# Kernel optimization log

Measured on AMD Instinct MI355X. Metric: run time of the kernel, lower is better.

The kernel has to match this reference:

```python
import jax, jax.numpy as jnp
import numpy as np

ALPHA = 1.702   # GLU sigmoid scale
LIMIT = 7.0     # clamp limit
K = 2           # experts per token


def setup_inputs() -> dict:
    key = jax.random.key(0)
    ks = jax.random.split(key, 4)
    B, S, H, E, I = 1, 1024, 1024, 8, 1024
    return {
        "hidden_states": jax.random.normal(ks[0], (B, S, H), jnp.float32),
        "router_weight": jax.random.normal(ks[1], (E, H), jnp.float32),
        "router_bias": jnp.zeros((E,), jnp.float32),
        "gate_up_proj": jax.random.normal(ks[2], (E, H, 2 * I), jnp.float32) * 0.02,
        "gate_up_bias": jnp.zeros((E, 2 * I), jnp.float32),
        "down_proj": jax.random.normal(ks[3], (E, I, H), jnp.float32) * 0.02,
        "down_bias": jnp.zeros((E, H), jnp.float32),
    }


def reference(hidden_states, router_weight, router_bias, gate_up_proj,
              gate_up_bias, down_proj, down_bias):
    B, S, H = hidden_states.shape
    E = router_weight.shape[0]
    I = down_proj.shape[1]
    T = B * S

    flat = hidden_states.reshape(T, H)

    # Router: softmax over experts, top-K selection (weights NOT renormalized).
    logits = flat @ router_weight.T + router_bias               # [T, E]
    scores = jax.nn.softmax(logits, axis=-1)
    topk_vals, topk_idx = jax.lax.top_k(scores, K)              # [T, K]

    # Dense per-token expert weight matrix (equivalent of dispatch metadata +
    # combine * topk_weights in the tt pipeline); top-k indices are unique.
    w = jnp.zeros((T, E), scores.dtype).at[
        jnp.arange(T)[:, None], topk_idx].set(topk_vals)        # [T, E]

    # Expert MLP with clamped GLU (gpt-oss style).
    gu = jnp.einsum('th,ehf->tef', flat, gate_up_proj) + gate_up_bias  # [T,E,2I]
    gate = jnp.minimum(gu[..., :I], LIMIT)
    up = jnp.clip(gu[..., I:], -LIMIT, LIMIT)
    glu = gate * jax.nn.sigmoid(gate * ALPHA)
    act = (up + 1.0) * glu                                       # [T, E, I]

    down = jnp.einsum('tei,eih->teh', act, down_proj) + down_bias  # [T, E, H]

    # Weighted combine over selected experts.
    out = jnp.einsum('teh,te->th', down, w)
    return out.reshape(B, S, H)
```

## Files before the change

kernel.cpp:

```cpp
#include <hip/hip_runtime.h>
#include <hip/hip_bf16.h>


typedef unsigned short u16;
typedef __attribute__((ext_vector_type(8))) __bf16 bf16x8;
typedef __attribute__((ext_vector_type(4))) float f32x4;

#define T_TOK 1024
#define H_DIM 1024
#define E_NUM 8
#define I_DIM 1024
#define ALPHA 1.702f
#define LIMIT 7.0f

__device__ __forceinline__ u16 f2bf(float f) {
    unsigned u = __builtin_bit_cast(unsigned, f);
    u = (u + 0x7FFFu + ((u >> 16) & 1u)) >> 16;
    return (u16)u;
}

__device__ __forceinline__ unsigned pk2(float lo, float hi) {
#if defined(__has_builtin) && __has_builtin(__builtin_amdgcn_cvt_pk_bf16_f32)
    typedef __attribute__((ext_vector_type(2))) __bf16 bf16x2_t;
    bf16x2_t v = __builtin_amdgcn_cvt_pk_bf16_f32(lo, hi);
    return __builtin_bit_cast(unsigned, v);
#else
    return (unsigned)f2bf(lo) | ((unsigned)f2bf(hi) << 16);
#endif
}

__device__ __forceinline__ f32x4 mfma16(bf16x8 a, bf16x8 b, f32x4 c) {
    return __builtin_amdgcn_mfma_f32_16x16x32_bf16(a, b, c, 0, 0, 0);
}

__device__ __forceinline__ void gld16(const void* g, void* l) {
    __builtin_amdgcn_global_load_lds(
        (const __attribute__((address_space(1))) void*)g,
        (__attribute__((address_space(3))) void*)l, 16, 0, 0);
}

__device__ __forceinline__ void expert_range(const int* counts, int e,
                                             int& cnt, int& abase) {
    int a = 0, c = 0;
#pragma unroll
    for (int i = 0; i < E_NUM; ++i) {
        int v = counts[i];
        if (i < e) a += v;
        if (i == e) c = v;
    }
    cnt = c; abase = a;
}

__global__ __launch_bounds__(256) void k_cvt(
    const float* __restrict__ gup, const float* __restrict__ dp,
    u16* __restrict__ gupT, u16* __restrict__ dpT, int* __restrict__ counts)
{
    if (blockIdx.x == 0 && threadIdx.x < E_NUM) counts[threadIdx.x] = 0;
    const int b = blockIdx.x;
    const float* src; u16* dst; int C, k0, c0;
    if (b < 4096) {
        int e = b >> 9, t = b & 511;
        k0 = (t >> 5) * 64; c0 = (t & 31) * 64;
        src = gup + ((size_t)e << 21); dst = gupT + ((size_t)e << 21); C = 2048;
    } else {
        int b2 = b - 4096;
        int e = b2 >> 8, t = b2 & 255;
        k0 = (t >> 4) * 64; c0 = (t & 15) * 64;
        src = dp + ((size_t)e << 20); dst = dpT + ((size_t)e << 20); C = 1024;
    }
    __shared__ u16 Ls[64][72];
    const int tid = threadIdx.x;
    const int rr = tid >> 4, cc = (tid & 15) * 4;
#pragma unroll
    for (int i = 0; i < 4; ++i) {
        int k = rr + i * 16;
        float4 v = *(const float4*)(src + (size_t)(k0 + k) * C + c0 + cc);
        Ls[cc + 0][k] = f2bf(v.x);
        Ls[cc + 1][k] = f2bf(v.y);
        Ls[cc + 2][k] = f2bf(v.z);
        Ls[cc + 3][k] = f2bf(v.w);
    }
    __syncthreads();
    const int oc = tid >> 2, och = (tid & 3) * 16;
    u16* orow = dst + (size_t)(c0 + oc) * 1024 + k0 + och;
    *(uint4*)(orow)     = *(uint4*)&Ls[oc][och];
    *(uint4*)(orow + 8) = *(uint4*)&Ls[oc][och + 8];
}

__global__ __launch_bounds__(256) void k_router(
    const float* __restrict__ x, const float* __restrict__ rw,
    const float* __restrict__ rb, const float* __restrict__ db,
    int* __restrict__ counts, int* __restrict__ tok_list,
    float* __restrict__ w_list, u16* __restrict__ xb,
    float* __restrict__ out)
{
    const int t = blockIdx.x;
    const int tid = threadIdx.x;
    const float4 xv = *(const float4*)(x + (size_t)t * H_DIM + tid * 4);

    *(uint2*)(xb + (size_t)t * H_DIM + tid * 4) =
        make_uint2(pk2(xv.x, xv.y), pk2(xv.z, xv.w));

    float p[E_NUM];
#pragma unroll
    for (int e = 0; e < E_NUM; ++e) {
        const float4 wv = *(const float4*)(rw + e * H_DIM + tid * 4);
        p[e] = xv.x * wv.x + xv.y * wv.y + xv.z * wv.z + xv.w * wv.w;
    }
#pragma unroll
    for (int off = 32; off; off >>= 1) {
#pragma unroll
        for (int e = 0; e < E_NUM; ++e) p[e] += __shfl_down(p[e], off, 64);
    }
    __shared__ float red[4][E_NUM];
    __shared__ int se[2];
    __shared__ float sw[2];
    const int lane = tid & 63, wvid = tid >> 6;
    if (lane == 0) {
#pragma unroll
        for (int e = 0; e < E_NUM; ++e) red[wvid][e] = p[e];
    }
    __syncthreads();
    if (tid == 0) {
        float lg[E_NUM];
#pragma unroll
        for (int e = 0; e < E_NUM; ++e)
            lg[e] = red[0][e] + red[1][e] + red[2][e] + red[3][e] + rb[e];
        float m1 = -1e30f, m2 = -1e30f; int i1 = 0, i2 = 0;
#pragma unroll
        for (int e = 0; e < E_NUM; ++e) {
            float l = lg[e];
            if (l > m1) { m2 = m1; i2 = i1; m1 = l; i1 = e; }
            else if (l > m2) { m2 = l; i2 = e; }
        }
        float s = 0.f;
#pragma unroll
        for (int e = 0; e < E_NUM; ++e) s += __expf(lg[e] - m1);
        const float w0 = 1.0f / s;
        const float w1 = __expf(m2 - m1) / s;
        int slot0 = atomicAdd(&counts[i1], 1);
        tok_list[i1 * T_TOK + slot0] = t;
        w_list[i1 * T_TOK + slot0] = w0;
        int slot1 = atomicAdd(&counts[i2], 1);
        tok_list[i2 * T_TOK + slot1] = t;
        w_list[i2 * T_TOK + slot1] = w1;
        se[0] = i1; se[1] = i2; sw[0] = w0; sw[1] = w1;
    }
    __syncthreads();
    const int e0 = se[0], e1 = se[1];
    const float w0 = sw[0], w1 = sw[1];
    const int c = tid * 4;
    float4 d0 = *(const float4*)(db + e0 * H_DIM + c);
    float4 d1 = *(const float4*)(db + e1 * H_DIM + c);
    float4 o;
    o.x = w0 * d0.x + w1 * d1.x;
    o.y = w0 * d0.y + w1 * d1.y;
    o.z = w0 * d0.z + w1 * d1.z;
    o.w = w0 * d0.w + w1 * d1.w;
    *(float4*)(out + (size_t)t * H_DIM + c) = o;
}

__global__ __launch_bounds__(256, 4) void k_gateup(
    const u16* __restrict__ gupT, const float* __restrict__ gub,
    const int* __restrict__ counts, const int* __restrict__ tok_list,
    const u16* __restrict__ xb, u16* __restrict__ act)
{
    const int e = blockIdx.z;
    int cnt, abase;
    expert_range(counts, e, cnt, abase);
    const int m0 = blockIdx.y * 64;
    if (m0 >= cnt) return;
    const int n0 = blockIdx.x * 32;
    const int tid = threadIdx.x;
    const int lane = tid & 63, wv = tid >> 6;
    const int fm = lane & 15, kg = lane >> 4;
    const int wm = wv >> 1, wn = wv & 1;

    __shared__ __align__(16) u16 As0[64 * 64], As1[64 * 64];
    __shared__ __align__(16) u16 Bs0[64 * 64], Bs1[64 * 64];

    const int lr = lane >> 3, lk = (lane & 7) * 8;
    const u16* gA[2];
#pragma unroll
    for (int i = 0; i < 2; ++i) {
        int row = (wv * 2 + i) * 8 + lr;
        int slot = m0 + row;
        int tok = (slot < cnt) ? tok_list[e * T_TOK + slot] : 0;
        gA[i] = xb + (size_t)tok * H_DIM + lk;
    }
    const u16* gB[2];
#pragma unroll
    for (int i = 0; i < 2; ++i) {
        int row = (wv * 2 + i) * 8 + lr;
        int col = (row < 32) ? (n0 + row) : (1024 + n0 + row - 32);
        gB[i] = gupT + ((size_t)e << 21) + (size_t)col * 1024 + lk;
    }

    f32x4 accg[2], accu[2];
#pragma unroll
    for (int m = 0; m < 2; ++m) {
        accg[m] = (f32x4){0.f, 0.f, 0.f, 0.f};
        accu[m] = (f32x4){0.f, 0.f, 0.f, 0.f};
    }

#define GU_STAGE(AS, BS, KB)                                                   \
    {                                                                          \
        gld16(gA[0] + (KB), (u16*)(AS) + (wv * 2 + 0) * 512);                  \
        gld16(gA[1] + (KB), (u16*)(AS) + (wv * 2 + 1) * 512);                  \
        gld16(gB[0] + (KB), (u16*)(BS) + (wv * 2 + 0) * 512);                  \
        gld16(gB[1] + (KB), (u16*)(BS) + (wv * 2 + 1) * 512);                  \
    }
#define GU_MFMA(AS, BS)                                                        \
    {                                                                          \
        _Pragma("unroll")                                                      \
        for (int ks = 0; ks < 2; ++ks) {                                       \
            const int ko = ks * 32 + kg * 8;                                   \
            bf16x8 a0 = *(const bf16x8*)((const u16*)(AS) + (wm * 32 + fm) * 64 + ko);      \
            bf16x8 a1 = *(const bf16x8*)((const u16*)(AS) + (wm * 32 + 16 + fm) * 64 + ko); \
            bf16x8 bg = *(const bf16x8*)((const u16*)(BS) + (wn * 16 + fm) * 64 + ko);      \
            bf16x8 bu = *(const bf16x8*)((const u16*)(BS) + (32 + wn * 16 + fm) * 64 + ko); \
            accg[0] = mfma16(a0, bg, accg[0]);                                 \
            accu[0] = mfma16(a0, bu, accu[0]);                                 \
            accg[1] = mfma16(a1, bg, accg[1]);                                 \
            accu[1] = mfma16(a1, bu, accu[1]);                                 \
        }                                                                      \
    }

    GU_STAGE(As0, Bs0, 0);
    __syncthreads();
    for (int kb = 0; kb < H_DIM; kb += 128) {
        GU_STAGE(As1, Bs1, kb + 64);
        GU_MFMA(As0, Bs0);
        __syncthreads();
        if (kb + 128 < H_DIM) GU_STAGE(As0, Bs0, kb + 128);
        GU_MFMA(As1, Bs1);
        __syncthreads();
    }
#undef GU_STAGE
#undef GU_MFMA

#pragma unroll
    for (int m = 0; m < 2; ++m) {
#pragma unroll
        for (int r = 0; r < 4; ++r) {
            int row = wm * 32 + m * 16 + kg * 4 + r;
            int slot = m0 + row;
            if (slot >= cnt) continue;
            size_t arow = (size_t)(abase + slot) * I_DIM;
            int cn = n0 + wn * 16 + fm;
            float g = accg[m][r] + gub[e * 2048 + cn];
            float u = accu[m][r] + gub[e * 2048 + 1024 + cn];
            g = fminf(g, LIMIT);
            u = fminf(fmaxf(u, -LIMIT), LIMIT);
            float glu = g / (1.f + __expf(-ALPHA * g));
            act[arow + cn] = f2bf((u + 1.f) * glu);
        }
    }
}

__global__ __launch_bounds__(256, 4) void k_down(
    const u16* __restrict__ dpT,
    const int* __restrict__ counts, const int* __restrict__ tok_list,
    const float* __restrict__ w_list,
    const u16* __restrict__ act, float* __restrict__ out)
{
    const int e = blockIdx.z & 7, ks = blockIdx.z >> 3;
    int cnt, abase;
    expert_range(counts, e, cnt, abase);
    const int m0 = blockIdx.y * 64;
    if (m0 >= cnt) return;
    const int n0 = blockIdx.x * 64;
    const int tid = threadIdx.x;
    const int lane = tid & 63, wv = tid >> 6;
    const int fm = lane & 15, kg = lane >> 4;
    const int wm = wv >> 1, wn = wv & 1;

    __shared__ __align__(16) u16 As0[64 * 64], As1[64 * 64];
    __shared__ __align__(16) u16 Bs0[64 * 64], Bs1[64 * 64];

    const int lr = lane >> 3, lk = (lane & 7) * 8;
    const u16* gA[2];
    const u16* gB[2];
#pragma unroll
    for (int i = 0; i < 2; ++i) {
        int row = (wv * 2 + i) * 8 + lr;
        gA[i] = act + (size_t)(abase + m0 + row) * I_DIM + ks * 512 + lk;
        gB[i] = dpT + ((size_t)e << 20) + (size_t)(n0 + row) * 1024 + ks * 512 + lk;
    }

    f32x4 acc[2][2];
#pragma unroll
    for (int m = 0; m < 2; ++m)
#pragma unroll
        for (int n = 0; n < 2; ++n) acc[m][n] = (f32x4){0.f, 0.f, 0.f, 0.f};

#define DN_STAGE(AS, BS, KB)                                                   \
    {                                                                          \
        gld16(gA[0] + (KB), (u16*)(AS) + (wv * 2 + 0) * 512);                  \
        gld16(gA[1] + (KB), (u16*)(AS) + (wv * 2 + 1) * 512);                  \
        gld16(gB[0] + (KB), (u16*)(BS) + (wv * 2 + 0) * 512);                  \
        gld16(gB[1] + (KB), (u16*)(BS) + (wv * 2 + 1) * 512);                  \
    }
#define DN_MFMA(AS, BS)                                                        \
    {                                                                          \
        _Pragma("unroll")                                                      \
        for (int ks2 = 0; ks2 < 2; ++ks2) {                                    \
            const int ko = ks2 * 32 + kg * 8;                                  \
            bf16x8 a0 = *(const bf16x8*)((const u16*)(AS) + (wm * 32 + fm) * 64 + ko);      \
            bf16x8 a1 = *(const bf16x8*)((const u16*)(AS) + (wm * 32 + 16 + fm) * 64 + ko); \
            bf16x8 b0 = *(const bf16x8*)((const u16*)(BS) + (wn * 32 + fm) * 64 + ko);      \
            bf16x8 b1 = *(const bf16x8*)((const u16*)(BS) + (wn * 32 + 16 + fm) * 64 + ko); \
            acc[0][0] = mfma16(a0, b0, acc[0][0]);                             \
            acc[0][1] = mfma16(a0, b1, acc[0][1]);                             \
            acc[1][0] = mfma16(a1, b0, acc[1][0]);                             \
            acc[1][1] = mfma16(a1, b1, acc[1][1]);                             \
        }                                                                      \
    }

    DN_STAGE(As0, Bs0, 0);
    __syncthreads();
    for (int kb = 0; kb < 512; kb += 128) {
        DN_STAGE(As1, Bs1, kb + 64);
        DN_MFMA(As0, Bs0);
        __syncthreads();
        if (kb + 128 < 512) DN_STAGE(As0, Bs0, kb + 128);
        DN_MFMA(As1, Bs1);
        __syncthreads();
    }
#undef DN_STAGE
#undef DN_MFMA

#pragma unroll
    for (int m = 0; m < 2; ++m) {
#pragma unroll
        for (int r = 0; r < 4; ++r) {
            int row = wm * 32 + m * 16 + kg * 4 + r;
            int slot = m0 + row;
            if (slot >= cnt) continue;
            float wgt = w_list[e * T_TOK + slot];
            int tok = tok_list[e * T_TOK + slot];
            float* orow = out + (size_t)tok * H_DIM;
#pragma unroll
            for (int n = 0; n < 2; ++n) {
                int col = n0 + wn * 32 + n * 16 + fm;
                atomicAdd(orow + col, acc[m][n][r] * wgt);
            }
        }
    }
}

extern "C" void kernel_launch(void* const* d_in, const int* in_sizes, int n_in,
                              void* d_out, int out_size, void* d_ws, size_t ws_size,
                              hipStream_t stream) {
    const float* x   = (const float*)d_in[0];
    const float* rw  = (const float*)d_in[1];
    const float* rb  = (const float*)d_in[2];
    const float* gup = (const float*)d_in[3];
    const float* gub = (const float*)d_in[4];
    const float* dp  = (const float*)d_in[5];
    const float* db  = (const float*)d_in[6];
    float* out = (float*)d_out;

    char* ws = (char*)d_ws;
    int*   counts   = (int*)(ws);
    int*   tok_list = (int*)(ws + 64);
    float* w_list   = (float*)(ws + 64 + 32768);
    u16*   xb       = (u16*)(ws + 65600);
    u16*   act      = (u16*)(ws + 65600 + 2097152);
    u16*   gupT     = (u16*)(ws + 8388608);
    u16*   dpT      = (u16*)(ws + 41943040);

    k_cvt<<<6144, 256, 0, stream>>>(gup, dp, gupT, dpT, counts);
    k_router<<<T_TOK, 256, 0, stream>>>(x, rw, rb, db, counts, tok_list, w_list,
                                        xb, out);
    k_gateup<<<dim3(32, 16, 8), 256, 0, stream>>>(gupT, gub, counts, tok_list,
                                                  xb, act);
    k_down<<<dim3(16, 16, 16), 256, 0, stream>>>(dpT, counts, tok_list, w_list,
                                                 act, out);
}
```

Before: 221.0 us.

## Widen gate-up tile, drop down-proj split-K, pack bf16 stores in convert

The gate-up kernel now computes 64 output columns per block instead of 32, which doubles the B tile and the accumulators and reuses each A fragment across more MFMAs. The launch grid is halved and the occupancy hint drops to 3. The down-projection kernel no longer splits K into two halves, so each block runs the full I reduction and fewer atomic adds hit the output. The weight-convert kernel reads four rows per thread and writes packed bf16 pairs as 8-byte shared stores instead of scalar 2-byte stores. The trade-off is lower parallelism in gate-up and down, and more registers and shared memory per block.

```diff
diff --git a/kernel.cpp b/kernel.cpp
--- a/kernel.cpp
+++ b/kernel.cpp
@@ -68,17 +68,19 @@
         k0 = (t >> 4) * 64; c0 = (t & 15) * 64;
         src = dp + ((size_t)e << 20); dst = dpT + ((size_t)e << 20); C = 1024;
     }
-    __shared__ u16 Ls[64][72];
+    __shared__ __align__(16) u16 Ls[64][72];
     const int tid = threadIdx.x;
-    const int rr = tid >> 4, cc = (tid & 15) * 4;
+    const int kq = tid >> 4, cq = tid & 15;
+    float4 v0 = *(const float4*)(src + (size_t)(k0 + kq * 4 + 0) * C + c0 + cq * 4);
+    float4 v1 = *(const float4*)(src + (size_t)(k0 + kq * 4 + 1) * C + c0 + cq * 4);
+    float4 v2 = *(const float4*)(src + (size_t)(k0 + kq * 4 + 2) * C + c0 + cq * 4);
+    float4 v3 = *(const float4*)(src + (size_t)(k0 + kq * 4 + 3) * C + c0 + cq * 4);
+    const float* p0 = (const float*)&v0; const float* p1 = (const float*)&v1;
+    const float* p2 = (const float*)&v2; const float* p3 = (const float*)&v3;
 #pragma unroll
     for (int i = 0; i < 4; ++i) {
-        int k = rr + i * 16;
-        float4 v = *(const float4*)(src + (size_t)(k0 + k) * C + c0 + cc);
-        Ls[cc + 0][k] = f2bf(v.x);
-        Ls[cc + 1][k] = f2bf(v.y);
-        Ls[cc + 2][k] = f2bf(v.z);
-        Ls[cc + 3][k] = f2bf(v.w);
+        *(uint2*)&Ls[cq * 4 + i][kq * 4] =
+            make_uint2(pk2(p0[i], p1[i]), pk2(p2[i], p3[i]));
     }
     __syncthreads();
     const int oc = tid >> 2, och = (tid & 3) * 16;
@@ -160,7 +162,7 @@
     *(float4*)(out + (size_t)t * H_DIM + c) = o;
 }
 
-__global__ __launch_bounds__(256, 4) void k_gateup(
+__global__ __launch_bounds__(256, 3) void k_gateup(
     const u16* __restrict__ gupT, const float* __restrict__ gub,
     const int* __restrict__ counts, const int* __restrict__ tok_list,
     const u16* __restrict__ xb, u16* __restrict__ act)
@@ -170,14 +172,14 @@
     expert_range(counts, e, cnt, abase);
     const int m0 = blockIdx.y * 64;
     if (m0 >= cnt) return;
-    const int n0 = blockIdx.x * 32;
+    const int n0 = blockIdx.x * 64;
     const int tid = threadIdx.x;
     const int lane = tid & 63, wv = tid >> 6;
     const int fm = lane & 15, kg = lane >> 4;
     const int wm = wv >> 1, wn = wv & 1;
 
     __shared__ __align__(16) u16 As0[64 * 64], As1[64 * 64];
-    __shared__ __align__(16) u16 Bs0[64 * 64], Bs1[64 * 64];
+    __shared__ __align__(16) u16 Bs0[128 * 64], Bs1[128 * 64];
 
     const int lr = lane >> 3, lk = (lane & 7) * 8;
     const u16* gA[2];
@@ -188,41 +190,51 @@
         int tok = (slot < cnt) ? tok_list[e * T_TOK + slot] : 0;
         gA[i] = xb + (size_t)tok * H_DIM + lk;
     }
-    const u16* gB[2];
-#pragma unroll
-    for (int i = 0; i < 2; ++i) {
-        int row = (wv * 2 + i) * 8 + lr;
-        int col = (row < 32) ? (n0 + row) : (1024 + n0 + row - 32);
+    const u16* gB[4];
+#pragma unroll
+    for (int i = 0; i < 4; ++i) {
+        int row = (wv * 4 + i) * 8 + lr;
+        int col = (row < 64) ? (n0 + row) : (1024 + n0 + row - 64);
         gB[i] = gupT + ((size_t)e << 21) + (size_t)col * 1024 + lk;
     }
 
-    f32x4 accg[2], accu[2];
-#pragma unroll
-    for (int m = 0; m < 2; ++m) {
-        accg[m] = (f32x4){0.f, 0.f, 0.f, 0.f};
-        accu[m] = (f32x4){0.f, 0.f, 0.f, 0.f};
-    }
+    f32x4 accg[2][2], accu[2][2];
+#pragma unroll
+    for (int m = 0; m < 2; ++m)
+#pragma unroll
+        for (int n = 0; n < 2; ++n) {
+            accg[m][n] = (f32x4){0.f, 0.f, 0.f, 0.f};
+            accu[m][n] = (f32x4){0.f, 0.f, 0.f, 0.f};
+        }
 
 #define GU_STAGE(AS, BS, KB)                                                   \
     {                                                                          \
         gld16(gA[0] + (KB), (u16*)(AS) + (wv * 2 + 0) * 512);                  \
         gld16(gA[1] + (KB), (u16*)(AS) + (wv * 2 + 1) * 512);                  \
-        gld16(gB[0] + (KB), (u16*)(BS) + (wv * 2 + 0) * 512);                  \
-        gld16(gB[1] + (KB), (u16*)(BS) + (wv * 2 + 1) * 512);                  \
+        gld16(gB[0] + (KB), (u16*)(BS) + (wv * 4 + 0) * 512);                  \
+        gld16(gB[1] + (KB), (u16*)(BS) + (wv * 4 + 1) * 512);                  \
+        gld16(gB[2] + (KB), (u16*)(BS) + (wv * 4 + 2) * 512);                  \
+        gld16(gB[3] + (KB), (u16*)(BS) + (wv * 4 + 3) * 512);                  \
     }
 #define GU_MFMA(AS, BS)                                                        \
     {                                                                          \
         _Pragma("unroll")                                                      \
         for (int ks = 0; ks < 2; ++ks) {                                       \
             const int ko = ks * 32 + kg * 8;                                   \
-            bf16x8 a0 = *(const bf16x8*)((const u16*)(AS) + (wm * 32 + fm) * 64 + ko);      \
-            bf16x8 a1 = *(const bf16x8*)((const u16*)(AS) + (wm * 32 + 16 + fm) * 64 + ko); \
-            bf16x8 bg = *(const bf16x8*)((const u16*)(BS) + (wn * 16 + fm) * 64 + ko);      \
-            bf16x8 bu = *(const bf16x8*)((const u16*)(BS) + (32 + wn * 16 + fm) * 64 + ko); \
-            accg[0] = mfma16(a0, bg, accg[0]);                                 \
-            accu[0] = mfma16(a0, bu, accu[0]);                                 \
-            accg[1] = mfma16(a1, bg, accg[1]);                                 \
-            accu[1] = mfma16(a1, bu, accu[1]);                                 \
+            bf16x8 a0 = *(const bf16x8*)((const u16*)(AS) + (wm * 32 + fm) * 64 + ko);        \
+            bf16x8 a1 = *(const bf16x8*)((const u16*)(AS) + (wm * 32 + 16 + fm) * 64 + ko);   \
+            bf16x8 bg0 = *(const bf16x8*)((const u16*)(BS) + (wn * 32 + fm) * 64 + ko);       \
+            bf16x8 bg1 = *(const bf16x8*)((const u16*)(BS) + (wn * 32 + 16 + fm) * 64 + ko);  \
+            bf16x8 bu0 = *(const bf16x8*)((const u16*)(BS) + (64 + wn * 32 + fm) * 64 + ko);  \
+            bf16x8 bu1 = *(const bf16x8*)((const u16*)(BS) + (64 + wn * 32 + 16 + fm) * 64 + ko); \
+            accg[0][0] = mfma16(a0, bg0, accg[0][0]);                          \
+            accg[0][1] = mfma16(a0, bg1, accg[0][1]);                          \
+            accu[0][0] = mfma16(a0, bu0, accu[0][0]);                          \
+            accu[0][1] = mfma16(a0, bu1, accu[0][1]);                          \
+            accg[1][0] = mfma16(a1, bg0, accg[1][0]);                          \
+            accg[1][1] = mfma16(a1, bg1, accg[1][1]);                          \
+            accu[1][0] = mfma16(a1, bu0, accu[1][0]);                          \
+            accu[1][1] = mfma16(a1, bu1, accu[1][1]);                          \
         }                                                                      \
     }
 
@@ -247,13 +259,16 @@
             int slot = m0 + row;
             if (slot >= cnt) continue;
             size_t arow = (size_t)(abase + slot) * I_DIM;
-            int cn = n0 + wn * 16 + fm;
-            float g = accg[m][r] + gub[e * 2048 + cn];
-            float u = accu[m][r] + gub[e * 2048 + 1024 + cn];
-            g = fminf(g, LIMIT);
-            u = fminf(fmaxf(u, -LIMIT), LIMIT);
-            float glu = g / (1.f + __expf(-ALPHA * g));
-            act[arow + cn] = f2bf((u + 1.f) * glu);
+#pragma unroll
+            for (int n = 0; n < 2; ++n) {
+                int cn = n0 + wn * 32 + n * 16 + fm;
+                float g = accg[m][n][r] + gub[e * 2048 + cn];
+                float u = accu[m][n][r] + gub[e * 2048 + 1024 + cn];
+                g = fminf(g, LIMIT);
+                u = fminf(fmaxf(u, -LIMIT), LIMIT);
+                float glu = g / (1.f + __expf(-ALPHA * g));
+                act[arow + cn] = f2bf((u + 1.f) * glu);
+            }
         }
     }
 }
@@ -264,7 +279,7 @@
     const float* __restrict__ w_list,
     const u16* __restrict__ act, float* __restrict__ out)
 {
-    const int e = blockIdx.z & 7, ks = blockIdx.z >> 3;
+    const int e = blockIdx.z;
     int cnt, abase;
     expert_range(counts, e, cnt, abase);
     const int m0 = blockIdx.y * 64;
@@ -284,8 +299,8 @@
 #pragma unroll
     for (int i = 0; i < 2; ++i) {
         int row = (wv * 2 + i) * 8 + lr;
-        gA[i] = act + (size_t)(abase + m0 + row) * I_DIM + ks * 512 + lk;
-        gB[i] = dpT + ((size_t)e << 20) + (size_t)(n0 + row) * 1024 + ks * 512 + lk;
+        gA[i] = act + (size_t)(abase + m0 + row) * I_DIM + lk;
+        gB[i] = dpT + ((size_t)e << 20) + (size_t)(n0 + row) * 1024 + lk;
     }
 
     f32x4 acc[2][2];
@@ -319,11 +334,11 @@
 
     DN_STAGE(As0, Bs0, 0);
     __syncthreads();
-    for (int kb = 0; kb < 512; kb += 128) {
+    for (int kb = 0; kb < I_DIM; kb += 128) {
         DN_STAGE(As1, Bs1, kb + 64);
         DN_MFMA(As0, Bs0);
         __syncthreads();
-        if (kb + 128 < 512) DN_STAGE(As0, Bs0, kb + 128);
+        if (kb + 128 < I_DIM) DN_STAGE(As0, Bs0, kb + 128);
         DN_MFMA(As1, Bs1);
         __syncthreads();
     }
@@ -373,8 +388,8 @@
     k_cvt<<<6144, 256, 0, stream>>>(gup, dp, gupT, dpT, counts);
     k_router<<<T_TOK, 256, 0, stream>>>(x, rw, rb, db, counts, tok_list, w_list,
                                         xb, out);
-    k_gateup<<<dim3(32, 16, 8), 256, 0, stream>>>(gupT, gub, counts, tok_list,
+    k_gateup<<<dim3(16, 16, 8), 256, 0, stream>>>(gupT, gub, counts, tok_list,
                                                   xb, act);
-    k_down<<<dim3(16, 16, 16), 256, 0, stream>>>(dpT, counts, tok_list, w_list,
-                                                 act, out);
-}
+    k_down<<<dim3(16, 16, 8), 256, 0, stream>>>(dpT, counts, tok_list, w_list,
+                                                act, out);
+}
```

New measurement: 216.1 us. -2.2%, faster.
